# Optimization experiments

Hardware: AMD Instinct MI355X
Metric: run time of the kernel (lower is better)

## Reference

```python
import math
import jax, jax.numpy as jnp
import numpy as np
from jax import lax

# Block_mamba(dim=192): x = x + Mamba(LN1(x)); x = x + EinFFT(LN2(x), H, W)
DIM = 192
D_STATE = 64
D_CONV = 4
EXPAND = 2
D_INNER = EXPAND * DIM          # 384
DT_RANK = math.ceil(DIM / 16)   # 12
NUM_BLOCKS = 4                  # EinFFT hardcoded
BLOCK_SIZE = DIM // NUM_BLOCKS  # 48
LAMBDA = 0.01                   # softshrink threshold


def setup_inputs() -> dict:
    key = jax.random.key(0)
    ks = jax.random.split(key, 20)
    B, N, C = 4, 1024, DIM
    s = 0.02
    x = jax.random.normal(ks[0], (B, N, C), jnp.float32)
    inp = {
        "x": x,
        "ln1_w": jnp.ones((C,), jnp.float32),
        "ln1_b": jnp.zeros((C,), jnp.float32),
        "in_proj_w": jax.random.normal(ks[1], (2 * D_INNER, C), jnp.float32) * s,
        "conv_w": jax.random.normal(ks[2], (D_INNER, 1, D_CONV), jnp.float32) * 0.1,
        "conv_b": jnp.zeros((D_INNER,), jnp.float32),
        "x_proj_w": jax.random.normal(ks[3], (DT_RANK + 2 * D_STATE, D_INNER), jnp.float32) * s,
        "dt_proj_w": jax.random.normal(ks[4], (D_INNER, DT_RANK), jnp.float32) * (DT_RANK ** -0.5),
        "dt_proj_b": jax.random.uniform(ks[5], (D_INNER,), jnp.float32, -4.0, -2.0),
        "A_log": jnp.log(jnp.broadcast_to(jnp.arange(1, D_STATE + 1, dtype=jnp.float32), (D_INNER, D_STATE))),
        "D": jnp.ones((D_INNER,), jnp.float32),
        "out_proj_w": jax.random.normal(ks[6], (C, D_INNER), jnp.float32) * s,
        "ln2_w": jnp.ones((C,), jnp.float32),
        "ln2_b": jnp.zeros((C,), jnp.float32),
        "cw1": jax.random.normal(ks[7], (2, NUM_BLOCKS, BLOCK_SIZE, BLOCK_SIZE), jnp.float32) * s,
        "cw2": jax.random.normal(ks[8], (2, NUM_BLOCKS, BLOCK_SIZE, BLOCK_SIZE), jnp.float32) * s,
        "cb1": jax.random.normal(ks[9], (2, NUM_BLOCKS, BLOCK_SIZE), jnp.float32) * s,
        "cb2": jax.random.normal(ks[10], (2, NUM_BLOCKS, BLOCK_SIZE), jnp.float32) * s,
        "H": 32,
        "W": 32,
    }
    return inp


def layer_norm(x, w, b, eps=1e-5):
    mu = jnp.mean(x, axis=-1, keepdims=True)
    var = jnp.var(x, axis=-1, keepdims=True)
    return (x - mu) * lax.rsqrt(var + eps) * w + b


def mamba(x, in_proj_w, conv_w, conv_b, x_proj_w, dt_proj_w, dt_proj_b, A_log, D):
    B, L, C = x.shape
    xz = jnp.einsum('blc,ec->ble', x, in_proj_w)          # [B,L,2*D_INNER]
    xm, z = jnp.split(xz, 2, axis=-1)                      # each [B,L,D_INNER]
    # causal depthwise conv1d (torch pads both sides then slices [:, :, :L])
    xc = lax.conv_general_dilated(
        xm.transpose(0, 2, 1), conv_w, (1,), [(D_CONV - 1, 0)],
        dimension_numbers=('NCH', 'OIH', 'NCH'), feature_group_count=D_INNER)
    xm = jax.nn.silu(xc + conv_b[None, :, None]).transpose(0, 2, 1)  # [B,L,D_INNER]
    dbc = jnp.einsum('bld,ed->ble', xm, x_proj_w)
    dt, Bm, Cm = jnp.split(dbc, [DT_RANK, DT_RANK + D_STATE], axis=-1)
    delta = jax.nn.softplus(jnp.einsum('blr,dr->bld', dt, dt_proj_w) + dt_proj_b)  # [B,L,D_INNER]
    A = -jnp.exp(A_log)                                    # [D_INNER, D_STATE]

    def step(h, inp):
        d_t, B_t, C_t, x_t = inp                           # [B,d],[B,n],[B,n],[B,d]
        dA = jnp.exp(d_t[:, :, None] * A)                  # [B,d,n]
        h = h * dA + (d_t * x_t)[:, :, None] * B_t[:, None, :]
        y = jnp.einsum('bdn,bn->bd', h, C_t)
        return h, y

    h0 = jnp.zeros((B, D_INNER, D_STATE), x.dtype)
    xs = (delta.transpose(1, 0, 2), Bm.transpose(1, 0, 2), Cm.transpose(1, 0, 2), xm.transpose(1, 0, 2))
    _, ys = lax.scan(step, h0, xs)                         # ys: [L,B,d]
    y = ys.transpose(1, 0, 2) + xm * D
    y = y * jax.nn.silu(z)
    return jnp.einsum('bld,cd->blc', y, out_proj_w_global[0])


# small trick to keep mamba signature tidy
out_proj_w_global = [None]


def einfft(x, cw1, cw2, cb1, cb2):
    B, N, C = x.shape
    xv = x.reshape(B, N, NUM_BLOCKS, BLOCK_SIZE)
    pad1 = (1 << math.ceil(math.log2(N))) - N
    pad2 = (1 << math.ceil(math.log2(NUM_BLOCKS))) - NUM_BLOCKS
    if pad1 or pad2:
        xv = jnp.pad(xv, ((0, 0), (0, pad1), (0, pad2), (0, 0)))
    X = jnp.fft.fft2(xv, axes=(1, 2), norm='ortho')
    mul = lambda t, w: jnp.einsum('Bnbd,bdk->Bnbk', t, w)
    r1 = jax.nn.relu(mul(X.real, cw1[0]) - mul(X.imag, cw1[1]) + cb1[0])
    i1 = jax.nn.relu(mul(X.real, cw1[1]) + mul(X.imag, cw1[0]) + cb1[1])
    r2 = mul(r1, cw2[0]) - mul(i1, cw2[1]) + cb2[0]
    i2 = mul(r1, cw2[1]) + mul(i1, cw2[0]) + cb2[1]
    ss = lambda v: jnp.where(v > LAMBDA, v - LAMBDA, jnp.where(v < -LAMBDA, v + LAMBDA, jnp.zeros((), v.dtype)))
    Z = ss(r2) + 1j * ss(i2)
    y = jnp.fft.ifft2(Z, axes=(1, 2), norm='ortho')[:, :N, :NUM_BLOCKS, :]
    return y.real.reshape(B, N, C)  # torch .to(real dtype) keeps real part


def reference(x, ln1_w, ln1_b, in_proj_w, conv_w, conv_b, x_proj_w, dt_proj_w, dt_proj_b,
              A_log, D, out_proj_w, ln2_w, ln2_b, cw1, cw2, cb1, cb2, H, W):
    out_proj_w_global[0] = out_proj_w
    x = x + mamba(layer_norm(x, ln1_w, ln1_b), in_proj_w, conv_w, conv_b,
                  x_proj_w, dt_proj_w, dt_proj_b, A_log, D)
    x = x + einfft(layer_norm(x, ln2_w, ln2_b), cw1, cw2, cb1, cb2)
    return x
```

## Files before the change

kernel.cpp:

```cpp
#include <hip/hip_runtime.h>
#include <math.h>

#define PI_F 3.14159265358979323846f

typedef __attribute__((ext_vector_type(8))) short short8v;
typedef __attribute__((ext_vector_type(4))) float f32x4;

__device__ __forceinline__ float lane_bcast(float v, int l) {
  return __int_as_float(__builtin_amdgcn_readlane(__float_as_int(v), l));
}

__device__ __forceinline__ unsigned short f2bf(float f) {
  unsigned u = __float_as_uint(f);
  unsigned r = u + 0x7FFFu + ((u >> 16) & 1u);
  return (unsigned short)(r >> 16);
}

__device__ __forceinline__ float wave_reduce_sum(float v) {
  v += __shfl_xor(v, 32, 64);
  v += __shfl_xor(v, 16, 64);
  v += __shfl_xor(v, 8, 64);
  v += __shfl_xor(v, 4, 64);
  v += __shfl_xor(v, 2, 64);
  v += __shfl_xor(v, 1, 64);
  return v;
}

__global__ __launch_bounds__(256) void ln_kernel(const float* __restrict__ x,
    const float* __restrict__ w, const float* __restrict__ b,
    const float* __restrict__ ipw, unsigned short* __restrict__ obf,
    unsigned short* __restrict__ wbf) {
  int row = blockIdx.x * 4 + (threadIdx.x >> 6);
  int lane = threadIdx.x & 63;
  const float* xr = x + (size_t)row * 192;
  float v0 = xr[lane], v1 = xr[lane + 64], v2 = xr[lane + 128];
  float s  = wave_reduce_sum(v0 + v1 + v2);
  float s2 = wave_reduce_sum(v0 * v0 + v1 * v1 + v2 * v2);
  float mu  = s * (1.f / 192.f);
  float var = s2 * (1.f / 192.f) - mu * mu;
  float rs  = rsqrtf(var + 1e-5f);
  unsigned short* orow = obf + (size_t)row * 192;
  orow[lane]       = f2bf((v0 - mu) * rs * w[lane]       + b[lane]);
  orow[lane + 64]  = f2bf((v1 - mu) * rs * w[lane + 64]  + b[lane + 64]);
  orow[lane + 128] = f2bf((v2 - mu) * rs * w[lane + 128] + b[lane + 128]);
  for (int i = threadIdx.x; i < 144; i += 256) {
    int idx = blockIdx.x * 144 + i;
    wbf[idx] = f2bf(ipw[idx]);
  }
}

__global__ __launch_bounds__(256) void gemm_mfma_in(
    const unsigned short* __restrict__ Abf, const unsigned short* __restrict__ Wbf,
    float* __restrict__ C) {
  int wave = threadIdx.x >> 6;
  int lane = threadIdx.x & 63;
  int m0 = blockIdx.y * 64 + wave * 16;
  int n0 = blockIdx.x * 64;
  int rw = lane & 15;
  int g  = lane >> 4;
  const unsigned short* Ap = Abf + (size_t)(m0 + rw) * 192 + g * 8;
  const unsigned short* Wp = Wbf + (size_t)(n0 + rw) * 192 + g * 8;
  f32x4 acc[4];
#pragma unroll
  for (int f = 0; f < 4; ++f) acc[f] = (f32x4){0.f, 0.f, 0.f, 0.f};
#pragma unroll
  for (int kk = 0; kk < 192; kk += 32) {
    short8v a = *(const short8v*)(Ap + kk);
#pragma unroll
    for (int f = 0; f < 4; ++f) {
      short8v bfr = *(const short8v*)(Wp + (size_t)f * 16 * 192 + kk);
      acc[f] = __builtin_amdgcn_mfma_f32_16x16x32_bf16(a, bfr, acc[f], 0, 0, 0);
    }
  }
#pragma unroll
  for (int f = 0; f < 4; ++f)
#pragma unroll
    for (int r = 0; r < 4; ++r)
      C[(size_t)(m0 + g * 4 + r) * 768 + n0 + f * 16 + rw] = acc[f][r];
}

__global__ __launch_bounds__(256) void gemm_mfma_xp(
    const unsigned short* __restrict__ Abf, const unsigned short* __restrict__ Wbf,
    float* __restrict__ C) {
  int wave = threadIdx.x >> 6;
  int lane = threadIdx.x & 63;
  int m0 = blockIdx.y * 64 + wave * 16;
  int n0 = blockIdx.x * 64;
  int rw = lane & 15;
  int g  = lane >> 4;
  const unsigned short* Ap = Abf + (size_t)(m0 + rw) * 384 + g * 8;
  f32x4 acc[4];
#pragma unroll
  for (int f = 0; f < 4; ++f) acc[f] = (f32x4){0.f, 0.f, 0.f, 0.f};
  short8v bz = {0, 0, 0, 0, 0, 0, 0, 0};
#pragma unroll
  for (int kk = 0; kk < 384; kk += 32) {
    short8v a = *(const short8v*)(Ap + kk);
#pragma unroll
    for (int f = 0; f < 4; ++f) {
      int n = n0 + f * 16 + rw;
      short8v bfr = (n < 140)
        ? *(const short8v*)(Wbf + (size_t)n * 384 + g * 8 + kk) : bz;
      acc[f] = __builtin_amdgcn_mfma_f32_16x16x32_bf16(a, bfr, acc[f], 0, 0, 0);
    }
  }
#pragma unroll
  for (int f = 0; f < 4; ++f)
#pragma unroll
    for (int r = 0; r < 4; ++r) {
      int n = n0 + f * 16 + rw;
      if (n < 140)
        C[(size_t)(m0 + g * 4 + r) * 140 + n] = acc[f][r];
    }
}

__global__ __launch_bounds__(256) void gemm_at32m(const float* __restrict__ AT,
    const unsigned short* __restrict__ Wbf, const float* __restrict__ res,
    float* __restrict__ C) {
  __shared__ unsigned As[64][17];
  int tid = threadIdx.x;
  int wave = tid >> 6, lane = tid & 63;
  int n0 = blockIdx.x * 64;
  int m0 = blockIdx.y * 64;
  int bb = m0 >> 10;
  int t0 = m0 & 1023;
  const float* Ab = AT + ((size_t)bb * 384) * 1024 + t0;
  int col = tid & 63;
  int kq  = tid >> 6;
  int rw = lane & 15, g = lane >> 4;
  f32x4 acc[4];
#pragma unroll
  for (int f = 0; f < 4; ++f) acc[f] = (f32x4){0.f, 0.f, 0.f, 0.f};
#pragma unroll
  for (int kk = 0; kk < 384; kk += 32) {
#pragma unroll
    for (int p = 0; p < 4; ++p) {
      int k2 = kq + p * 4;
      int k = kk + k2 * 2;
      float f0 = Ab[(size_t)k * 1024 + col];
      float f1 = Ab[(size_t)(k + 1) * 1024 + col];
      As[col][k2] = (unsigned)f2bf(f0) | ((unsigned)f2bf(f1) << 16);
    }
    __syncthreads();
    int mrow = wave * 16 + rw;
    unsigned u0 = As[mrow][g * 4 + 0];
    unsigned u1 = As[mrow][g * 4 + 1];
    unsigned u2 = As[mrow][g * 4 + 2];
    unsigned u3 = As[mrow][g * 4 + 3];
    short8v a;
    ((unsigned*)&a)[0] = u0; ((unsigned*)&a)[1] = u1;
    ((unsigned*)&a)[2] = u2; ((unsigned*)&a)[3] = u3;
#pragma unroll
    for (int f = 0; f < 4; ++f) {
      short8v bfr = *(const short8v*)(Wbf + (size_t)(n0 + f * 16 + rw) * 384 + kk + g * 8);
      acc[f] = __builtin_amdgcn_mfma_f32_16x16x32_bf16(a, bfr, acc[f], 0, 0, 0);
    }
    __syncthreads();
  }
#pragma unroll
  for (int f = 0; f < 4; ++f)
#pragma unroll
    for (int r = 0; r < 4; ++r) {
      int m = m0 + wave * 16 + g * 4 + r;
      int n = n0 + f * 16 + rw;
      C[(size_t)m * 192 + n] = acc[f][r] + res[(size_t)m * 192 + n];
    }
}

__global__ __launch_bounds__(256) void ln2t_kernel(const float* __restrict__ x,
    const float* __restrict__ w, const float* __restrict__ b, float* __restrict__ xT) {
  __shared__ float xt[32][193];
  __shared__ float mu_s[32], rs_s[32];
  int blk = blockIdx.x;
  int Bi = blk >> 5;
  int t0 = (blk & 31) * 32;
  int tid = threadIdx.x;
  const float* xb = x + ((size_t)(Bi * 1024 + t0)) * 192;
  for (int i = tid; i < 32 * 192; i += 256) {
    xt[i / 192][i % 192] = xb[i];
  }
  __syncthreads();
  int row = tid >> 3, seg = tid & 7;
  float s = 0.f, s2 = 0.f;
  const float* xr = &xt[row][seg * 24];
#pragma unroll
  for (int k = 0; k < 24; ++k) { float v = xr[k]; s += v; s2 += v * v; }
  s  += __shfl_xor(s, 1, 64);  s  += __shfl_xor(s, 2, 64);  s  += __shfl_xor(s, 4, 64);
  s2 += __shfl_xor(s2, 1, 64); s2 += __shfl_xor(s2, 2, 64); s2 += __shfl_xor(s2, 4, 64);
  if (seg == 0) {
    float mu = s * (1.f / 192.f);
    float var = s2 * (1.f / 192.f) - mu * mu;
    mu_s[row] = mu;
    rs_s[row] = rsqrtf(var + 1e-5f);
  }
  __syncthreads();
  for (int i = tid; i < 32 * 192; i += 256) {
    int ch = i >> 5, r2 = i & 31;
    float v = (xt[r2][ch] - mu_s[r2]) * rs_s[r2] * w[ch] + b[ch];
    xT[((size_t)(Bi * 192 + ch)) * 1024 + t0 + r2] = v;
  }
}

__global__ __launch_bounds__(256) void conv_silu(const float* __restrict__ xz,
    const float* __restrict__ cw, const float* __restrict__ cb,
    float* __restrict__ xc, unsigned short* __restrict__ xcbf,
    const float* __restrict__ xpw, unsigned short* __restrict__ xpwbf) {
  if (threadIdx.x < 35) {
    int ci = blockIdx.x * 35 + threadIdx.x;
    xpwbf[ci] = f2bf(xpw[ci]);
  }
  int e4 = blockIdx.x * 256 + threadIdx.x;
  if (e4 >= 4 * 1024 * 96) return;
  int d4 = e4 % 96;
  int t  = (e4 / 96) % 1024;
  int b  = e4 / (96 * 1024);
  int d = d4 * 4;
  const float* base = xz + (size_t)(b * 1024) * 768 + d;
  float4 acc = *(const float4*)(cb + d);
  const float4* cwv = (const float4*)(cw + d * 4);
  float4 c0 = cwv[0], c1 = cwv[1], c2 = cwv[2], c3 = cwv[3];
#pragma unroll
  for (int j = 0; j < 4; ++j) {
    int tt = t - 3 + j;
    if (tt >= 0) {
      float4 v = *(const float4*)(base + (size_t)tt * 768);
      float w0 = (&c0.x)[j], w1 = (&c1.x)[j], w2 = (&c2.x)[j], w3 = (&c3.x)[j];
      acc.x = fmaf(v.x, w0, acc.x);
      acc.y = fmaf(v.y, w1, acc.y);
      acc.z = fmaf(v.z, w2, acc.z);
      acc.w = fmaf(v.w, w3, acc.w);
    }
  }
  float4 o;
  o.x = acc.x / (1.f + __expf(-acc.x));
  o.y = acc.y / (1.f + __expf(-acc.y));
  o.z = acc.z / (1.f + __expf(-acc.z));
  o.w = acc.w / (1.f + __expf(-acc.w));
  size_t idx = ((size_t)(b * 1024 + t) * 384) + d;
  *(float4*)(xc + idx) = o;
  uint2 pk;
  pk.x = (unsigned)f2bf(o.x) | ((unsigned)f2bf(o.y) << 16);
  pk.y = (unsigned)f2bf(o.z) | ((unsigned)f2bf(o.w) << 16);
  *(uint2*)(xcbf + idx) = pk;
}

__global__ __launch_bounds__(256) void delta_trans(const float* __restrict__ dbc,
    const float* __restrict__ dtw, const float* __restrict__ dtb,
    const float* __restrict__ xc, float* __restrict__ dltT, float* __restrict__ duT,
    const float* __restrict__ opw, unsigned short* __restrict__ opwbf) {
  __shared__ float dts[64][13];
  __shared__ float xt[64][65];
  int blk = blockIdx.x;
  int b  = blk / 96;
  int rem = blk % 96;
  int tt = rem / 6, dd = rem % 6;
  int t0 = tt * 64, d0 = dd * 64;
  int tid = threadIdx.x;
  for (int i = tid; i < 192; i += 256) {
    int idx = blk * 192 + i;
    opwbf[idx] = f2bf(opw[idx]);
  }
  for (int i = tid; i < 64 * 12; i += 256) {
    int tl = i / 12, r = i % 12;
    dts[tl][r] = dbc[((size_t)b * 1024 + t0 + tl) * 140 + r];
  }
  {
    int col = tid & 63, rg = tid >> 6;
#pragma unroll
    for (int j = 0; j < 16; ++j) {
      int row = j * 4 + rg;
      xt[row][col] = xc[((size_t)b * 1024 + t0 + row) * 384 + d0 + col];
    }
  }
  __syncthreads();
  int tl = tid & 63, grp = tid >> 6;
#pragma unroll
  for (int j = 0; j < 16; ++j) {
    int dl = grp * 16 + j;
    int d = d0 + dl;
    float s = dtb[d];
#pragma unroll
    for (int r = 0; r < 12; ++r) s += dts[tl][r] * dtw[d * 12 + r];
    float dlt = (s > 20.f) ? s : log1pf(__expf(s));
    size_t ob = ((size_t)b * 384 + d) * 1024 + t0 + tl;
    dltT[ob] = dlt;
    duT[ob]  = dlt * xt[tl][dl];
  }
}

#define SCAN_GBODY(G, BC, CC, XCV, ZVV, BN, CN, XCN, ZVN)                  \
  {                                                                        \
    int ts_ = (G) * 16;                                                    \
    if ((G) + 1 < 64) {                                                    \
      int tn_ = ts_ + 16;                                                  \
      _Pragma("unroll")                                                    \
      for (int i = 0; i < 16; ++i) {                                       \
        size_t ro = (size_t)(tn_ + i) * 140;                               \
        BN[i] = Bp[ro]; CN[i] = Cp[ro];                                    \
      }                                                                    \
      if (lane < 16) { XCN = xcp[(size_t)(tn_ + lane) * 384];              \
                       ZVN = xzp[(size_t)(tn_ + lane) * 768]; }            \
      if (((G) & 3) == 2) {                                                \
        int sn_ = ((G) >> 2) + 1;                                          \
        if (sn_ < 16) { dvN = dT[sn_ * 64 + lane];                         \
                        duN = uT[sn_ * 64 + lane]; }                       \
      }                                                                    \
    }                                                                      \
    int tb_ = ts_ & 63;                                                    \
    _Pragma("unroll")                                                      \
    for (int i = 0; i < 16; ++i) {                                         \
      float sdv = lane_bcast(dvC, tb_ + i);                                \
      float sdu = lane_bcast(duC, tb_ + i);                                \
      float a = exp2f(sdv * A);                                            \
      h = fmaf(h, a, sdu * BC[i]);                                         \
      tile[i][lane] = h * CC[i];                                           \
    }                                                                      \
    const float* trow_ = &tile[tq][q * 16];                                \
    float s_ = 0.f;                                                        \
    _Pragma("unroll")                                                      \
    for (int i = 0; i < 16; ++i) s_ += trow_[i];                           \
    s_ += __shfl_xor(s_, 16, 64);                                          \
    s_ += __shfl_xor(s_, 32, 64);                                          \
    if (lane < 16) {                                                       \
      float sg_ = ZVV / (1.f + __expf(-ZVV));                              \
      yp[ts_ + lane] = (s_ + XCV * ddv) * sg_;                             \
    }                                                                      \
    if (((G) & 3) == 3) { dvC = dvN; duC = duN; }                          \
  }

__global__ __launch_bounds__(64, 1) void scan_single(const float* __restrict__ dltT,
    const float* __restrict__ duT, const float* __restrict__ dbc,
    const float* __restrict__ A_log, const float* __restrict__ xc,
    const float* __restrict__ xz, const float* __restrict__ Dvec,
    float* __restrict__ yT) {
  __shared__ float tile[16][65];
  int bd = blockIdx.x;
  int b = bd / 384, d = bd % 384;
  int lane = threadIdx.x;
  float A = -__expf(A_log[d * 64 + lane]) * 1.44269504f;
  const float* dT = dltT + ((size_t)b * 384 + d) * 1024;
  const float* uT = duT  + ((size_t)b * 384 + d) * 1024;
  const float* Bp = dbc + ((size_t)b * 1024) * 140 + 12 + lane;
  const float* Cp = Bp + 64;
  float ddv = Dvec[d];
  float* yp = yT + ((size_t)b * 384 + d) * 1024;
  const float* xcp = xc + ((size_t)b * 1024) * 384 + d;
  const float* xzp = xz + ((size_t)b * 1024) * 768 + 384 + d;
  int tq = lane & 15;
  int q  = lane >> 4;
  float h = 0.f;

  float Ba[16], Ca[16], Bb[16], Cb[16];
  float dvC, duC, dvN = 0.f, duN = 0.f;
  float xcA = 0.f, zvA = 0.f, xcB = 0.f, zvB = 0.f;

  dvC = dT[lane];
  duC = uT[lane];
#pragma unroll
  for (int i = 0; i < 16; ++i) {
    size_t ro = (size_t)i * 140;
    Ba[i] = Bp[ro];
    Ca[i] = Cp[ro];
  }
  if (lane < 16) {
    xcA = xcp[(size_t)lane * 384];
    zvA = xzp[(size_t)lane * 768];
  }

  for (int gp = 0; gp < 32; ++gp) {
    int g0 = gp * 2;
    SCAN_GBODY(g0,     Ba, Ca, xcA, zvA, Bb, Cb, xcB, zvB)
    SCAN_GBODY(g0 + 1, Bb, Cb, xcB, zvB, Ba, Ca, xcA, zvA)
  }
}

__device__ __forceinline__ int rev4_10(int i) {
  unsigned r = __brev((unsigned)i) >> 22;
  return (int)(((r & 0x155u) << 1) | ((r >> 1) & 0x155u));
}

__device__ __forceinline__ void fft1024r4(float* __restrict__ re,
    float* __restrict__ im, const float* __restrict__ twc,
    const float* __restrict__ tws, int tid, float sgn) {
  for (int i = tid; i < 1024; i += 256) {
    int r = rev4_10(i);
    if (i < r) {
      float t = re[i]; re[i] = re[r]; re[r] = t;
      t = im[i]; im[i] = im[r]; im[r] = t;
    }
  }
  __syncthreads();
  {
    float4 ar = *(float4*)&re[tid * 4];
    float4 ai = *(float4*)&im[tid * 4];
    float apc_r = ar.x + ar.z, amc_r = ar.x - ar.z;
    float apc_i = ai.x + ai.z, amc_i = ai.x - ai.z;
    float bpd_r = ar.y + ar.w, bmd_r = ar.y - ar.w;
    float bpd_i = ai.y + ai.w, bmd_i = ai.y - ai.w;
    float4 yr, yi;
    yr.x = apc_r + bpd_r;        yi.x = apc_i + bpd_i;
    yr.z = apc_r - bpd_r;        yi.z = apc_i - bpd_i;
    yr.y = amc_r - sgn * bmd_i;  yi.y = amc_i + sgn * bmd_r;
    yr.w = amc_r + sgn * bmd_i;  yi.w = amc_i - sgn * bmd_r;
    *(float4*)&re[tid * 4] = yr;
    *(float4*)&im[tid * 4] = yi;
  }
  __syncthreads();
#pragma unroll
  for (int s = 1; s < 5; ++s) {
    int L = 1 << (2 * s);
    int tstep = 256 >> (2 * s);
    int j = tid & (L - 1);
    int base = ((tid >> (2 * s)) << (2 * s + 2)) + j;
    int i0 = base, i1 = base + L, i2 = base + 2 * L, i3 = base + 3 * L;
    int x1i = j * tstep;
    float w1c = twc[x1i],     w1s = tws[x1i];
    float w2c = twc[2 * x1i], w2s = tws[2 * x1i];
    float w3c = twc[3 * x1i], w3s = tws[3 * x1i];
    float ar_ = re[i0], ai_ = im[i0];
    float br_ = re[i1], bi_ = im[i1];
    float cr_ = re[i2], ci_ = im[i2];
    float dr_ = re[i3], di_ = im[i3];
    float tbr = br_ * w1c - bi_ * w1s, tbi = br_ * w1s + bi_ * w1c;
    float tcr = cr_ * w2c - ci_ * w2s, tci = cr_ * w2s + ci_ * w2c;
    float tdr = dr_ * w3c - di_ * w3s, tdi = dr_ * w3s + di_ * w3c;
    float apc_r = ar_ + tcr, amc_r = ar_ - tcr;
    float apc_i = ai_ + tci, amc_i = ai_ - tci;
    float bpd_r = tbr + tdr, bmd_r = tbr - tdr;
    float bpd_i = tbi + tdi, bmd_i = tbi - tdi;
    re[i0] = apc_r + bpd_r;       im[i0] = apc_i + bpd_i;
    re[i2] = apc_r - bpd_r;       im[i2] = apc_i - bpd_i;
    re[i1] = amc_r - sgn * bmd_i; im[i1] = amc_i + sgn * bmd_r;
    re[i3] = amc_r + sgn * bmd_i; im[i3] = amc_i - sgn * bmd_r;
    __syncthreads();
  }
}

__global__ __launch_bounds__(256) void fft_fwd(const float* __restrict__ x2T,
    float* __restrict__ Xre, float* __restrict__ Xim) {
  __shared__ float re[1024];
  __shared__ float im[1024];
  __shared__ float twc[768];
  __shared__ float tws[768];
  int blk = blockIdx.x;
  int unit = blk & 1;
  int rest = blk >> 1;
  int d = rest % 48, Bi = rest / 48;
  int tid = threadIdx.x;
  for (int k = tid; k < 768; k += 256) {
    float sv, cv;
    __sincosf(-PI_F * (float)k * (1.f / 512.f), &sv, &cv);
    twc[k] = cv; tws[k] = sv;
  }
  const float* pb = x2T + ((size_t)(Bi * 192 + d)) * 1024;
  for (int n = tid; n < 1024; n += 256) {
    float v0 = pb[n];
    float v1 = pb[48 * 1024 + n];
    float v2 = pb[96 * 1024 + n];
    float v3 = pb[144 * 1024 + n];
    float rr, ii;
    if (unit == 0) { rr = v0 + v1 + v2 + v3; ii = v0 - v1 + v2 - v3; }
    else           { rr = v0 - v2;           ii = -(v1 - v3); }
    re[n] = rr; im[n] = ii;
  }
  __syncthreads();
  fft1024r4(re, im, twc, tws, tid, -1.0f);
  if (unit == 0) {
    float* r0 = Xre + ((size_t)((Bi * 4 + 0) * 48 + d)) * 1024;
    float* i0 = Xim + ((size_t)((Bi * 4 + 0) * 48 + d)) * 1024;
    float* r2 = Xre + ((size_t)((Bi * 4 + 2) * 48 + d)) * 1024;
    float* i2 = Xim + ((size_t)((Bi * 4 + 2) * 48 + d)) * 1024;
    for (int k = tid; k < 1024; k += 256) {
      int nk = (1024 - k) & 1023;
      float zr = re[k], zi = im[k];
      float yr = re[nk], yi = im[nk];
      r0[k] = (zr + yr) * (0.5f / 64.f);
      i0[k] = (zi - yi) * (0.5f / 64.f);
      r2[k] = (zi + yi) * (0.5f / 64.f);
      i2[k] = (yr - zr) * (0.5f / 64.f);
    }
  } else {
    float* r1 = Xre + ((size_t)((Bi * 4 + 1) * 48 + d)) * 1024;
    float* i1 = Xim + ((size_t)((Bi * 4 + 1) * 48 + d)) * 1024;
    float* r3 = Xre + ((size_t)((Bi * 4 + 3) * 48 + d)) * 1024;
    float* i3 = Xim + ((size_t)((Bi * 4 + 3) * 48 + d)) * 1024;
    for (int k = tid; k < 1024; k += 256) {
      int nk = (1024 - k) & 1023;
      r1[k] = re[k] * (1.f / 64.f);
      i1[k] = im[k] * (1.f / 64.f);
      r3[k] = re[nk] * (1.f / 64.f);
      i3[k] = -im[nk] * (1.f / 64.f);
    }
  }
}

__global__ __launch_bounds__(256) void mix_fused(float* __restrict__ Xre,
    float* __restrict__ Xim, const float* __restrict__ cw1,
    const float* __restrict__ cw2, const float* __restrict__ cb1,
    const float* __restrict__ cb2) {
  __shared__ float r1s[4][48][4];
  __shared__ float i1s[4][48][4];
  int w = threadIdx.x >> 6;
  int j = threadIdx.x & 63;
  int rg = blockIdx.x * 4 + w;
  int kq = rg & 255;
  int b  = (rg >> 8) & 3;
  int Bi = rg >> 10;
  int k0 = kq * 4;
  size_t xbase = ((size_t)((Bi * 4 + b) * 48)) * 1024 + k0;
  if (j < 48) {
    const float* wr = cw1 + b * 2304;
    const float* wi = cw1 + 9216 + b * 2304;
    float b1r = cb1[b * 48 + j], b1i = cb1[192 + b * 48 + j];
    float ar[4] = {b1r, b1r, b1r, b1r};
    float ai[4] = {b1i, b1i, b1i, b1i};
#pragma unroll 8
    for (int dd = 0; dd < 48; ++dd) {
      float4 xr = *(const float4*)(Xre + xbase + (size_t)dd * 1024);
      float4 xi = *(const float4*)(Xim + xbase + (size_t)dd * 1024);
      float wrv = wr[dd * 48 + j], wiv = wi[dd * 48 + j];
      ar[0] = fmaf(xr.x, wrv, ar[0]); ar[0] = fmaf(-xi.x, wiv, ar[0]);
      ai[0] = fmaf(xr.x, wiv, ai[0]); ai[0] = fmaf(xi.x, wrv, ai[0]);
      ar[1] = fmaf(xr.y, wrv, ar[1]); ar[1] = fmaf(-xi.y, wiv, ar[1]);
      ai[1] = fmaf(xr.y, wiv, ai[1]); ai[1] = fmaf(xi.y, wrv, ai[1]);
      ar[2] = fmaf(xr.z, wrv, ar[2]); ar[2] = fmaf(-xi.z, wiv, ar[2]);
      ai[2] = fmaf(xr.z, wiv, ai[2]); ai[2] = fmaf(xi.z, wrv, ai[2]);
      ar[3] = fmaf(xr.w, wrv, ar[3]); ar[3] = fmaf(-xi.w, wiv, ar[3]);
      ai[3] = fmaf(xr.w, wiv, ai[3]); ai[3] = fmaf(xi.w, wrv, ai[3]);
    }
    float4 r1v, i1v;
    r1v.x = fmaxf(ar[0], 0.f); r1v.y = fmaxf(ar[1], 0.f);
    r1v.z = fmaxf(ar[2], 0.f); r1v.w = fmaxf(ar[3], 0.f);
    i1v.x = fmaxf(ai[0], 0.f); i1v.y = fmaxf(ai[1], 0.f);
    i1v.z = fmaxf(ai[2], 0.f); i1v.w = fmaxf(ai[3], 0.f);
    *(float4*)&r1s[w][j][0] = r1v;
    *(float4*)&i1s[w][j][0] = i1v;
    const float* wr2 = cw2 + b * 2304;
    const float* wi2 = cw2 + 9216 + b * 2304;
    float b2r = cb2[b * 48 + j], b2i = cb2[192 + b * 48 + j];
    float a2r[4] = {b2r, b2r, b2r, b2r};
    float a2i[4] = {b2i, b2i, b2i, b2i};
#pragma unroll 8
    for (int dd = 0; dd < 48; ++dd) {
      float4 rv = *(const float4*)&r1s[w][dd][0];
      float4 iv = *(const float4*)&i1s[w][dd][0];
      float wrv = wr2[dd * 48 + j], wiv = wi2[dd * 48 + j];
      a2r[0] = fmaf(rv.x, wrv, a2r[0]); a2r[0] = fmaf(-iv.x, wiv, a2r[0]);
      a2i[0] = fmaf(rv.x, wiv, a2i[0]); a2i[0] = fmaf(iv.x, wrv, a2i[0]);
      a2r[1] = fmaf(rv.y, wrv, a2r[1]); a2r[1] = fmaf(-iv.y, wiv, a2r[1]);
      a2i[1] = fmaf(rv.y, wiv, a2i[1]); a2i[1] = fmaf(iv.y, wrv, a2i[1]);
      a2r[2] = fmaf(rv.z, wrv, a2r[2]); a2r[2] = fmaf(-iv.z, wiv, a2r[2]);
      a2i[2] = fmaf(rv.z, wiv, a2i[2]); a2i[2] = fmaf(iv.z, wrv, a2i[2]);
      a2r[3] = fmaf(rv.w, wrv, a2r[3]); a2r[3] = fmaf(-iv.w, wiv, a2r[3]);
      a2i[3] = fmaf(rv.w, wiv, a2i[3]); a2i[3] = fmaf(iv.w, wrv, a2i[3]);
    }
    float4 zr, zi;
#pragma unroll
    for (int r = 0; r < 4; ++r) {
      float vr = a2r[r], vi = a2i[r];
      (&zr.x)[r] = (vr > 0.01f) ? vr - 0.01f : ((vr < -0.01f) ? vr + 0.01f : 0.f);
      (&zi.x)[r] = (vi > 0.01f) ? vi - 0.01f : ((vi < -0.01f) ? vi + 0.01f : 0.f);
    }
    size_t obase = ((size_t)((Bi * 4 + b) * 48 + j)) * 1024 + k0;
    *(float4*)(Xre + obase) = zr;
    *(float4*)(Xim + obase) = zi;
  }
}

__global__ __launch_bounds__(256) void fft_inv(const float* __restrict__ Zre,
    const float* __restrict__ Zim, const float* __restrict__ x1, float* __restrict__ out) {
  __shared__ float re[1024];
  __shared__ float im[1024];
  __shared__ float twc[768];
  __shared__ float tws[768];
  int blk = blockIdx.x;
  int c = blk & 3;
  int rest = blk >> 2;
  int d = rest % 48, Bi = rest / 48;
  int tid = threadIdx.x;
  for (int k = tid; k < 768; k += 256) {
    float sv, cv;
    __sincosf(PI_F * (float)k * (1.f / 512.f), &sv, &cv);
    twc[k] = cv; tws[k] = sv;
  }
  const float* zr0 = Zre + ((size_t)((Bi * 4) * 48 + d)) * 1024;
  const float* zi0 = Zim + ((size_t)((Bi * 4) * 48 + d)) * 1024;
  const int cs = 48 * 1024;
  for (int k = tid; k < 1024; k += 256) {
    float r0 = zr0[k], r1v = zr0[cs + k], r2 = zr0[2 * cs + k], r3 = zr0[3 * cs + k];
    float i0 = zi0[k], i1v = zi0[cs + k], i2 = zi0[2 * cs + k], i3 = zi0[3 * cs + k];
    float rr, ii;
    if (c == 0)      { rr = r0 + r1v + r2 + r3;  ii = i0 + i1v + i2 + i3; }
    else if (c == 1) { rr = r0 - i1v - r2 + i3;  ii = i0 + r1v - i2 - r3; }
    else if (c == 2) { rr = r0 - r1v + r2 - r3;  ii = i0 - i1v + i2 - i3; }
    else             { rr = r0 + i1v - r2 - i3;  ii = i0 - r1v - i2 + r3; }
    re[k] = rr; im[k] = ii;
  }
  __syncthreads();
  fft1024r4(re, im, twc, tws, tid, 1.0f);
  for (int n = tid; n < 1024; n += 256) {
    size_t o = (size_t)(Bi * 1024 + n) * 192 + c * 48 + d;
    out[o] = x1[o] + re[n] * (1.f / 64.f);
  }
}

extern "C" void kernel_launch(void* const* d_in, const int* in_sizes, int n_in,
                              void* d_out, int out_size, void* d_ws, size_t ws_size,
                              hipStream_t stream) {
  const float* x         = (const float*)d_in[0];
  const float* ln1_w     = (const float*)d_in[1];
  const float* ln1_b     = (const float*)d_in[2];
  const float* in_proj_w = (const float*)d_in[3];
  const float* conv_w    = (const float*)d_in[4];
  const float* conv_b    = (const float*)d_in[5];
  const float* x_proj_w  = (const float*)d_in[6];
  const float* dt_proj_w = (const float*)d_in[7];
  const float* dt_proj_b = (const float*)d_in[8];
  const float* A_log     = (const float*)d_in[9];
  const float* Dvec      = (const float*)d_in[10];
  const float* out_proj_w= (const float*)d_in[11];
  const float* ln2_w     = (const float*)d_in[12];
  const float* ln2_b     = (const float*)d_in[13];
  const float* cw1       = (const float*)d_in[14];
  const float* cw2       = (const float*)d_in[15];
  const float* cb1       = (const float*)d_in[16];
  const float* cb2       = (const float*)d_in[17];
  float* out = (float*)d_out;
  float* ws  = (float*)d_ws;

  float* xz   = ws;
  float* xc   = xz  + 3145728;
  float* dbc  = xc  + 1572864;
  float* dltT = dbc + 573440;
  float* yvT  = dltT + 1572864;
  float* xln  = yvT + 1572864;
  float* x2T  = xln + 786432;
  float* Xre  = x2T + 786432;
  float* Xim  = Xre + 786432;
  float* duT = Xre;
  float* x1 = xln;
  unsigned short* xbf = (unsigned short*)(Xim + 786432);
  unsigned short* wbf = (unsigned short*)(Xim + 786432 + 393216);
  unsigned short* opwbf = (unsigned short*)(Xim + 786432 + 393216 + 36864);
  unsigned short* xcbf  = (unsigned short*)xln;
  unsigned short* xpwbf = (unsigned short*)x2T;

  ln_kernel<<<1024, 256, 0, stream>>>(x, ln1_w, ln1_b, in_proj_w, xbf, wbf);
  gemm_mfma_in<<<dim3(12, 64), 256, 0, stream>>>(xbf, wbf, xz);
  conv_silu<<<1536, 256, 0, stream>>>(xz, conv_w, conv_b, xc, xcbf, x_proj_w, xpwbf);
  gemm_mfma_xp<<<dim3(3, 64), 256, 0, stream>>>(xcbf, xpwbf, dbc);
  delta_trans<<<384, 256, 0, stream>>>(dbc, dt_proj_w, dt_proj_b, xc, dltT, duT,
                                       out_proj_w, opwbf);
  scan_single<<<1536, 64, 0, stream>>>(dltT, duT, dbc, A_log, xc, xz, Dvec, yvT);
  gemm_at32m<<<dim3(3, 64), 256, 0, stream>>>(yvT, opwbf, x, x1);
  ln2t_kernel<<<128, 256, 0, stream>>>(x1, ln2_w, ln2_b, x2T);
  fft_fwd<<<384, 256, 0, stream>>>(x2T, Xre, Xim);
  mix_fused<<<1024, 256, 0, stream>>>(Xre, Xim, cw1, cw2, cb1, cb2);
  fft_inv<<<768, 256, 0, stream>>>(Xre, Xim, x1, out);
}
```

Before: 291.6 us.

## Pack two real-output inverse FFTs into one complex FFT via Hermitian split

The inverse FFT kernel now computes two output columns per block by forming the Hermitian-symmetric parts of two spectra, combining them as A + iB, and running a single complex 1024-point FFT whose real and imaginary parts give the two real outputs. This halves the number of blocks and FFTs, since only the real part of each inverse transform is needed. It adds a second mirrored gather per element (reads at index -k) and extra arithmetic, and it relies on taking only the real part being equivalent to symmetrizing.

New measurement: 293.0 us. About the same (+0.5%).

```diff
diff --git a/kernel.cpp b/kernel.cpp
--- a/kernel.cpp
+++ b/kernel.cpp
@@ -574,8 +574,8 @@
   __shared__ float twc[768];
   __shared__ float tws[768];
   int blk = blockIdx.x;
-  int c = blk & 3;
-  int rest = blk >> 2;
+  int unit = blk & 1;
+  int rest = blk >> 1;
   int d = rest % 48, Bi = rest / 48;
   int tid = threadIdx.x;
   for (int k = tid; k < 768; k += 256) {
@@ -587,20 +587,35 @@
   const float* zi0 = Zim + ((size_t)((Bi * 4) * 48 + d)) * 1024;
   const int cs = 48 * 1024;
   for (int k = tid; k < 1024; k += 256) {
-    float r0 = zr0[k], r1v = zr0[cs + k], r2 = zr0[2 * cs + k], r3 = zr0[3 * cs + k];
-    float i0 = zi0[k], i1v = zi0[cs + k], i2 = zi0[2 * cs + k], i3 = zi0[3 * cs + k];
-    float rr, ii;
-    if (c == 0)      { rr = r0 + r1v + r2 + r3;  ii = i0 + i1v + i2 + i3; }
-    else if (c == 1) { rr = r0 - i1v - r2 + i3;  ii = i0 + r1v - i2 - r3; }
-    else if (c == 2) { rr = r0 - r1v + r2 - r3;  ii = i0 - i1v + i2 - i3; }
-    else             { rr = r0 + i1v - r2 - i3;  ii = i0 - r1v - i2 + r3; }
-    re[k] = rr; im[k] = ii;
+    int nk = (1024 - k) & 1023;
+    float r0 = zr0[k],  r1v = zr0[cs + k],  r2 = zr0[2 * cs + k],  r3 = zr0[3 * cs + k];
+    float i0 = zi0[k],  i1v = zi0[cs + k],  i2 = zi0[2 * cs + k],  i3 = zi0[3 * cs + k];
+    float s0 = zr0[nk], s1 = zr0[cs + nk], s2 = zr0[2 * cs + nk], s3 = zr0[3 * cs + nk];
+    float j0 = zi0[nk], j1 = zi0[cs + nk], j2 = zi0[2 * cs + nk], j3 = zi0[3 * cs + nk];
+    float ar, ai, br, bi, anr, ani, bnr, bni;
+    if (unit == 0) {
+      ar  = r0 + r1v + r2 + r3;  ai  = i0 + i1v + i2 + i3;
+      br  = r0 - i1v - r2 + i3;  bi  = i0 + r1v - i2 - r3;
+      anr = s0 + s1 + s2 + s3;   ani = j0 + j1 + j2 + j3;
+      bnr = s0 - j1 - s2 + j3;   bni = j0 + s1 - j2 - s3;
+    } else {
+      ar  = r0 - r1v + r2 - r3;  ai  = i0 - i1v + i2 - i3;
+      br  = r0 + i1v - r2 - i3;  bi  = i0 - r1v - i2 + r3;
+      anr = s0 - s1 + s2 - s3;   ani = j0 - j1 + j2 - j3;
+      bnr = s0 + j1 - s2 - j3;   bni = j0 - s1 - j2 + s3;
+    }
+    float Har = 0.5f * (ar + anr), Hai = 0.5f * (ai - ani);
+    float Hbr = 0.5f * (br + bnr), Hbi = 0.5f * (bi - bni);
+    re[k] = Har - Hbi;
+    im[k] = Hai + Hbr;
   }
   __syncthreads();
   fft1024r4(re, im, twc, tws, tid, 1.0f);
+  int c0 = unit * 2;
   for (int n = tid; n < 1024; n += 256) {
-    size_t o = (size_t)(Bi * 1024 + n) * 192 + c * 48 + d;
-    out[o] = x1[o] + re[n] * (1.f / 64.f);
+    size_t o = (size_t)(Bi * 1024 + n) * 192 + c0 * 48 + d;
+    out[o]      = x1[o]      + re[n] * (1.f / 64.f);
+    out[o + 48] = x1[o + 48] + im[n] * (1.f / 64.f);
   }
 }
 
@@ -656,5 +671,5 @@
   ln2t_kernel<<<128, 256, 0, stream>>>(x1, ln2_w, ln2_b, x2T);
   fft_fwd<<<384, 256, 0, stream>>>(x2T, Xre, Xim);
   mix_fused<<<1024, 256, 0, stream>>>(Xre, Xim, cw1, cw2, cb1, cb2);
-  fft_inv<<<768, 256, 0, stream>>>(Xre, Xim, x1, out);
-}
+  fft_inv<<<384, 256, 0, stream>>>(Xre, Xim, x1, out);
+}
```
